# Kernel tuning notes

Measured on AMD Instinct MI355X. Metric: run time of the kernel, lower is better.

The kernel has to match this reference:

```python
import jax, jax.numpy as jnp
import numpy as np

N = 2_000_000   # num_nodes
C = 128         # in_channels
B = 256         # num graphs
K = 32          # max branches per graph (branch ids in [0, K))
NEG_SLOPE = 0.01  # torch leaky_relu default


def setup_inputs() -> dict:
    key = jax.random.key(0)
    k1, k2, k3, k4, k5, k6 = jax.random.split(key, 6)
    node_embed = jax.random.normal(k1, (N, C), dtype=jnp.float32)
    batch = jnp.sort(jax.random.randint(k2, (N,), 0, B, dtype=jnp.int64))
    branch = jax.random.randint(k3, (N,), 0, K, dtype=jnp.int64)
    s1 = 1.0 / np.sqrt(C)
    W1 = jax.random.uniform(k4, (C, C), jnp.float32, -s1, s1)
    b1 = jnp.zeros((C,), jnp.float32)
    W2 = jax.random.uniform(k5, (C, 1), jnp.float32, -s1, s1)
    b2 = jnp.zeros((1,), jnp.float32)
    return {"node_embed": node_embed, "batch": batch, "branch": branch,
            "W1": W1, "b1": b1, "W2": W2, "b2": b2}


def reference(node_embed, batch, branch, W1, b1, W2, b2):
    # Original code compacts branch ids via per-graph offsets (cumsum of max+1).
    # Equivalent static-shape formulation: global slot id = batch*K + branch,
    # and a per-graph mask keeping slots b <= max(branch in graph) — exactly the
    # branches 0..num_branch_per_graph-1 that repeat_interleave covers (including
    # empty branches below the max, whose pooled embed is 0 -> MLP(0)).
    gid = batch * K + branch                               # [N]
    branch_embed = jax.ops.segment_sum(node_embed, gid, num_segments=B * K)  # [B*K, C]
    h = branch_embed @ W1 + b1
    h = jnp.where(h >= 0, h, NEG_SLOPE * h)                # leaky_relu
    branch_value = h @ W2 + b2                             # [B*K, 1]
    max_b = jax.ops.segment_max(branch, batch, num_segments=B)  # [B]
    mask = (jnp.arange(K)[None, :] <= max_b[:, None]).astype(branch_value.dtype)  # [B, K]
    graph_value = jnp.sum(branch_value.reshape(B, K) * mask, axis=1, keepdims=True)  # [B, 1]
    return graph_value
```

## Files before the change

kernel.cpp:

```cpp
#include <hip/hip_runtime.h>

#define NCH 128
#define NGR 256
#define NBR 32
#define NEG_SLOPE 0.01f

typedef __attribute__((ext_vector_type(8))) short bf16x8;
typedef __attribute__((ext_vector_type(4))) float f32x4;

constexpr int TROWS = 32;

__device__ inline unsigned short rtne_bf16(float x) {
    unsigned u = __float_as_uint(x);
    return (unsigned short)((u + 0x7FFFu + ((u >> 16) & 1u)) >> 16);
}
__device__ inline unsigned pack_hl(float v) {
    const unsigned u = __float_as_uint(v);
    const unsigned short h = (unsigned short)(u >> 16);
    const float hf = __uint_as_float(u & 0xFFFF0000u);
    const unsigned short l = rtne_bf16(v - hf);
    return ((unsigned)h << 16) | (unsigned)l;
}

__global__ __launch_bounds__(512, 4) void scatter_mfma(
    const float* __restrict__ node_embed,
    const int*   __restrict__ batch,
    const int*   __restrict__ branch,
    float*       __restrict__ part,
    int*         __restrict__ max_b_part,
    int n_nodes)
{
    __shared__ float buf[3][TROWS][NCH] __attribute__((aligned(16)));
    __shared__ int   sbr_i[3][64]       __attribute__((aligned(16)));
    __shared__ int   seg_s[2];
    __shared__ int   wm[8];

    const int t    = threadIdx.x;
    const int bid  = blockIdx.x;
    const int g    = bid >> 1;
    const int half = bid & 1;
    const int wave = t >> 6;
    const int lane = t & 63;
    const int c    = wave;
    const int gq   = lane >> 4;
    const int m    = lane & 15;

    if (t < 2) {
        const int target = g + t;
        int lo = 0, hi = n_nodes;
        while (lo < hi) { int mid = (lo + hi) >> 1; if (batch[mid] < target) lo = mid + 1; else hi = mid; }
        seg_s[t] = lo;
    }
    __syncthreads();
    const int s0 = seg_s[0], s1 = seg_s[1];
    const int nt_tot = (s1 - s0 + TROWS - 1) / TROWS;
    const int ntA    = (nt_tot + 1) >> 1;
    const int sa     = half ? s0 + ntA * TROWS : s0;
    const int nt     = half ? nt_tot - ntA : ntA;

    auto stage = [&](int ti, int bi) {
        const int c0n = sa + ti * TROWS;
        #pragma unroll
        for (int u = 0; u < 2; ++u) {
            const int koff = (u * 8 + wave) * 1024;
            const int lanebyte = koff + lane * 16;
            const int rowg = c0n + (lanebyte >> 9);
            const char* src = (const char*)node_embed + ((size_t)c0n * 512 + (size_t)lanebyte);
            if (rowg >= s1) src = (const char*)node_embed;
            __builtin_amdgcn_global_load_lds(
                (const __attribute__((address_space(1))) void*)src,
                (__attribute__((address_space(3))) void*)((char*)&buf[bi][0][0] + koff),
                16, 0, 0);
        }
        if (wave == 0) {
            const int i0 = min(c0n + lane, n_nodes - 1);
            __builtin_amdgcn_global_load_lds(
                (const __attribute__((address_space(1))) void*)(branch + i0),
                (__attribute__((address_space(3))) void*)((char*)&sbr_i[bi][0]), 4, 0, 0);
        }
    };

    f32x4 acc0 = {0.f, 0.f, 0.f, 0.f};
    f32x4 acc1 = {0.f, 0.f, 0.f, 0.f};
    int mymax = -1;

    auto compute = [&](int ti, int bi) {
        const int rem = s1 - (sa + ti * TROWS);
        const int4 i0 = *(const int4*)&sbr_i[bi][gq * 8];
        const int4 i1 = *(const int4*)&sbr_i[bi][gq * 8 + 4];
        const int idv[8] = {i0.x, i0.y, i0.z, i0.w, i1.x, i1.y, i1.z, i1.w};
        bf16x8 a0, a1, bh, bl;
        #pragma unroll
        for (int j = 0; j < 8; ++j) {
            const float v = buf[bi][gq * 8 + j][c * 16 + m];
            const unsigned u = __float_as_uint(v);
            bh[j] = (short)(unsigned short)(u >> 16);
            const float hf = __uint_as_float(u & 0xFFFF0000u);
            bl[j] = (short)rtne_bf16(v - hf);
            const bool val = (gq * 8 + j) < rem;
            a0[j] = (val && idv[j] == m)      ? (short)0x3F80 : (short)0;
            a1[j] = (val && idv[j] == m + 16) ? (short)0x3F80 : (short)0;
            if (val) mymax = max(mymax, idv[j]);
        }
        acc0 = __builtin_amdgcn_mfma_f32_16x16x32_bf16(a0, bh, acc0, 0, 0, 0);
        acc0 = __builtin_amdgcn_mfma_f32_16x16x32_bf16(a0, bl, acc0, 0, 0, 0);
        acc1 = __builtin_amdgcn_mfma_f32_16x16x32_bf16(a1, bh, acc1, 0, 0, 0);
        acc1 = __builtin_amdgcn_mfma_f32_16x16x32_bf16(a1, bl, acc1, 0, 0, 0);
    };

    if (nt > 0) {
        stage(0, 0);
        if (nt > 1) stage(1, 1);
        if (nt > 1) {
            if (wave == 0) asm volatile("s_waitcnt vmcnt(3)" ::: "memory");
            else           asm volatile("s_waitcnt vmcnt(2)" ::: "memory");
        } else {
            asm volatile("s_waitcnt vmcnt(0)" ::: "memory");
        }
        __builtin_amdgcn_s_barrier();
        __builtin_amdgcn_sched_barrier(0);

        for (int ti = 0; ti < nt; ++ti) {
            const int bi = ti % 3;
            if (ti + 2 < nt) stage(ti + 2, (ti + 2) % 3);
            const int k = min(nt - 1 - ti, 2);
            if (wave == 0) {
                if (k == 2)      asm volatile("s_waitcnt vmcnt(6)" ::: "memory");
                else if (k == 1) asm volatile("s_waitcnt vmcnt(3)" ::: "memory");
                else             asm volatile("s_waitcnt vmcnt(0)" ::: "memory");
            } else {
                if (k == 2)      asm volatile("s_waitcnt vmcnt(4)" ::: "memory");
                else if (k == 1) asm volatile("s_waitcnt vmcnt(2)" ::: "memory");
                else             asm volatile("s_waitcnt vmcnt(0)" ::: "memory");
            }
            __builtin_amdgcn_s_barrier();
            __builtin_amdgcn_sched_barrier(0);
            compute(ti, bi);
            __builtin_amdgcn_s_barrier();
            __builtin_amdgcn_sched_barrier(0);
        }
    }

    {
        const int sr = gq * 4;
        float* be = part + (size_t)half * NGR * NBR * NCH
                  + (size_t)g * NBR * NCH + (size_t)c * 16 + m;
        #pragma unroll
        for (int r = 0; r < 4; ++r) {
            be[(sr + r) * NCH]      = acc0[r];
            be[(16 + sr + r) * NCH] = acc1[r];
        }
    }

    int v = mymax;
    #pragma unroll
    for (int off = 32; off > 0; off >>= 1) v = max(v, __shfl_down(v, off));
    if (lane == 0) wm[wave] = v;
    __syncthreads();
    if (t == 0) {
        int mb = wm[0];
        #pragma unroll
        for (int i = 1; i < 8; ++i) mb = max(mb, wm[i]);
        max_b_part[half * NGR + g] = mb;
    }
}

__global__ __launch_bounds__(512) void mlp_mfma(
    const float* __restrict__ part,
    const int*   __restrict__ max_b_part,
    const float* __restrict__ W1,
    const float* __restrict__ b1,
    const float* __restrict__ W2,
    const float* __restrict__ b2,
    float*       __restrict__ out)
{
    __shared__ unsigned w1p[128 * 130];
    __shared__ unsigned epk[32 * 132];
    __shared__ float    red[32 * 8];

    const int t    = threadIdx.x;
    const int g    = blockIdx.x;
    const int wave = t >> 6;
    const int lane = t & 63;
    const int gq   = lane >> 4;
    const int m    = lane & 15;
    const int sh   = wave & 1;
    const int c0   = wave >> 1;

    #pragma unroll
    for (int i = 0; i < 8; ++i) {
        const int eb  = i * 2048 + t * 4;
        const int row = eb >> 7, col = eb & 127;
        const float4 w = *(const float4*)&W1[eb];
        unsigned* d = &w1p[row * 130 + col];
        *(uint2*)d       = make_uint2(pack_hl(w.x), pack_hl(w.y));
        *(uint2*)(d + 2) = make_uint2(pack_hl(w.z), pack_hl(w.w));
    }
    {
        const int slot = t >> 4, kb = (t & 15) * 8;
        const size_t base = ((size_t)g * NBR + slot) * NCH + kb;
        const float* pB = part + (size_t)NGR * NBR * NCH;
        float4 e0 = *(const float4*)&part[base];
        float4 e1 = *(const float4*)&part[base + 4];
        const float4 f0 = *(const float4*)&pB[base];
        const float4 f1 = *(const float4*)&pB[base + 4];
        e0.x += f0.x; e0.y += f0.y; e0.z += f0.z; e0.w += f0.w;
        e1.x += f1.x; e1.y += f1.y; e1.z += f1.z; e1.w += f1.w;
        unsigned* d = &epk[slot * 132 + kb];
        *(uint4*)d       = make_uint4(pack_hl(e0.x), pack_hl(e0.y), pack_hl(e0.z), pack_hl(e0.w));
        *(uint4*)(d + 4) = make_uint4(pack_hl(e1.x), pack_hl(e1.y), pack_hl(e1.z), pack_hl(e1.w));
    }
    const float b1v0 = b1[c0 * 16 + m],      b1v1 = b1[(c0 + 4) * 16 + m];
    const float w2v0 = W2[c0 * 16 + m],      w2v1 = W2[(c0 + 4) * 16 + m];
    __syncthreads();

    f32x4 accA = {0.f, 0.f, 0.f, 0.f};
    f32x4 accB = {0.f, 0.f, 0.f, 0.f};
    #pragma unroll
    for (int ks = 0; ks < 4; ++ks) {
        const int k0 = ks * 32;
        const unsigned* ap = &epk[(sh * 16 + m) * 132 + k0 + gq * 8];
        const uint4 aw0 = *(const uint4*)ap;
        const uint4 aw1 = *(const uint4*)(ap + 4);
        const unsigned aw[8] = {aw0.x, aw0.y, aw0.z, aw0.w, aw1.x, aw1.y, aw1.z, aw1.w};
        bf16x8 ah, al;
        #pragma unroll
        for (int j = 0; j < 8; ++j) { ah[j] = (short)(aw[j] >> 16); al[j] = (short)(aw[j] & 0xFFFFu); }

        bf16x8 bh, blo;
        #pragma unroll
        for (int j = 0; j < 8; ++j) {
            const unsigned w = w1p[(k0 + gq * 8 + j) * 130 + c0 * 16 + m];
            bh[j] = (short)(w >> 16); blo[j] = (short)(w & 0xFFFFu);
        }
        accA = __builtin_amdgcn_mfma_f32_16x16x32_bf16(ah, bh,  accA, 0, 0, 0);
        accA = __builtin_amdgcn_mfma_f32_16x16x32_bf16(al, bh,  accA, 0, 0, 0);
        accA = __builtin_amdgcn_mfma_f32_16x16x32_bf16(ah, blo, accA, 0, 0, 0);

        #pragma unroll
        for (int j = 0; j < 8; ++j) {
            const unsigned w = w1p[(k0 + gq * 8 + j) * 130 + (c0 + 4) * 16 + m];
            bh[j] = (short)(w >> 16); blo[j] = (short)(w & 0xFFFFu);
        }
        accB = __builtin_amdgcn_mfma_f32_16x16x32_bf16(ah, bh,  accB, 0, 0, 0);
        accB = __builtin_amdgcn_mfma_f32_16x16x32_bf16(al, bh,  accB, 0, 0, 0);
        accB = __builtin_amdgcn_mfma_f32_16x16x32_bf16(ah, blo, accB, 0, 0, 0);
    }

    #pragma unroll
    for (int r = 0; r < 4; ++r) {
        float h0 = accA[r] + b1v0;
        h0 = (h0 >= 0.f) ? h0 : NEG_SLOPE * h0;
        float s0v = h0 * w2v0;
        float h1 = accB[r] + b1v1;
        h1 = (h1 >= 0.f) ? h1 : NEG_SLOPE * h1;
        float s1v = h1 * w2v1;
        #pragma unroll
        for (int off = 1; off < 16; off <<= 1) {
            s0v += __shfl_xor(s0v, off);
            s1v += __shfl_xor(s1v, off);
        }
        if (m == 0) {
            const int slot = sh * 16 + gq * 4 + r;
            red[slot * 8 + c0]     = s0v;
            red[slot * 8 + c0 + 4] = s1v;
        }
    }
    __syncthreads();

    if (t < 64) {
        const int rr = lane & 31;
        float v = 0.f;
        #pragma unroll
        for (int cc = 0; cc < 8; ++cc) v += red[rr * 8 + cc];
        const int mb = max(max_b_part[g], max_b_part[NGR + g]);
        float val = (lane < 32 && rr <= mb) ? (v + b2[0]) : 0.f;
        #pragma unroll
        for (int off = 32; off > 0; off >>= 1) val += __shfl_down(val, off);
        if (t == 0) out[g] = val;
    }
}

extern "C" void kernel_launch(void* const* d_in, const int* in_sizes, int n_in,
                              void* d_out, int out_size, void* d_ws, size_t ws_size,
                              hipStream_t stream) {
    const float* node_embed = (const float*)d_in[0];
    const int*   batch      = (const int*)d_in[1];
    const int*   branch     = (const int*)d_in[2];
    const float* W1         = (const float*)d_in[3];
    const float* b1         = (const float*)d_in[4];
    const float* W2         = (const float*)d_in[5];
    const float* b2         = (const float*)d_in[6];
    float*       out        = (float*)d_out;

    const int n_nodes = in_sizes[0] / NCH;

    float* part = (float*)d_ws;
    int*   max_b_part = (int*)((char*)d_ws + 2 * (size_t)NGR * NBR * NCH * sizeof(float));

    scatter_mfma<<<2 * NGR, 512, 0, stream>>>(node_embed, batch, branch,
                                              part, max_b_part, n_nodes);
    mlp_mfma<<<NGR, 512, 0, stream>>>(part, max_b_part, W1, b1, W2, b2, out);
}
```

Measured before the change: 210.0 us.

## Split each graph across four blocks and use double buffering to raise occupancy

Each graph's node range is now split across four blocks instead of two, giving 1024 scatter blocks. The shared-memory ring drops from three stages to two so more blocks can be resident, and launch bounds now request 6 blocks per CU. The MLP kernel sums four partial slabs and four max partials. The risk is a shallower prefetch depth per block and extra partial-sum traffic in the second kernel.

Result: slower. 234.3 us (+11.5%).

```diff
diff --git a/kernel.cpp b/kernel.cpp
--- a/kernel.cpp
+++ b/kernel.cpp
@@ -9,6 +9,7 @@
 typedef __attribute__((ext_vector_type(4))) float f32x4;
 
 constexpr int TROWS = 32;
+constexpr int NSPLIT = 4;
 
 __device__ inline unsigned short rtne_bf16(float x) {
     unsigned u = __float_as_uint(x);
@@ -22,7 +23,7 @@
     return ((unsigned)h << 16) | (unsigned)l;
 }
 
-__global__ __launch_bounds__(512, 4) void scatter_mfma(
+__global__ __launch_bounds__(512, 6) void scatter_mfma(
     const float* __restrict__ node_embed,
     const int*   __restrict__ batch,
     const int*   __restrict__ branch,
@@ -30,15 +31,15 @@
     int*         __restrict__ max_b_part,
     int n_nodes)
 {
-    __shared__ float buf[3][TROWS][NCH] __attribute__((aligned(16)));
-    __shared__ int   sbr_i[3][64]       __attribute__((aligned(16)));
+    __shared__ float buf[2][TROWS][NCH] __attribute__((aligned(16)));
+    __shared__ int   sbr_i[2][64]       __attribute__((aligned(16)));
     __shared__ int   seg_s[2];
     __shared__ int   wm[8];
 
     const int t    = threadIdx.x;
     const int bid  = blockIdx.x;
-    const int g    = bid >> 1;
-    const int half = bid & 1;
+    const int g    = bid >> 2;
+    const int q    = bid & 3;
     const int wave = t >> 6;
     const int lane = t & 63;
     const int c    = wave;
@@ -54,9 +55,11 @@
     __syncthreads();
     const int s0 = seg_s[0], s1 = seg_s[1];
     const int nt_tot = (s1 - s0 + TROWS - 1) / TROWS;
-    const int ntA    = (nt_tot + 1) >> 1;
-    const int sa     = half ? s0 + ntA * TROWS : s0;
-    const int nt     = half ? nt_tot - ntA : ntA;
+    const int per    = (nt_tot + NSPLIT - 1) / NSPLIT;
+    const int t0     = q * per;
+    const int t1     = min(t0 + per, nt_tot);
+    const int nt     = max(t1 - t0, 0);
+    const int sa     = s0 + t0 * TROWS;
 
     auto stage = [&](int ti, int bi) {
         const int c0n = sa + ti * TROWS;
@@ -110,28 +113,14 @@
 
     if (nt > 0) {
         stage(0, 0);
-        if (nt > 1) stage(1, 1);
-        if (nt > 1) {
-            if (wave == 0) asm volatile("s_waitcnt vmcnt(3)" ::: "memory");
-            else           asm volatile("s_waitcnt vmcnt(2)" ::: "memory");
-        } else {
-            asm volatile("s_waitcnt vmcnt(0)" ::: "memory");
-        }
-        __builtin_amdgcn_s_barrier();
-        __builtin_amdgcn_sched_barrier(0);
-
         for (int ti = 0; ti < nt; ++ti) {
-            const int bi = ti % 3;
-            if (ti + 2 < nt) stage(ti + 2, (ti + 2) % 3);
-            const int k = min(nt - 1 - ti, 2);
-            if (wave == 0) {
-                if (k == 2)      asm volatile("s_waitcnt vmcnt(6)" ::: "memory");
-                else if (k == 1) asm volatile("s_waitcnt vmcnt(3)" ::: "memory");
-                else             asm volatile("s_waitcnt vmcnt(0)" ::: "memory");
+            const int bi = ti & 1;
+            if (ti + 1 < nt) stage(ti + 1, bi ^ 1);
+            if (ti + 1 < nt) {
+                if (wave == 0) asm volatile("s_waitcnt vmcnt(3)" ::: "memory");
+                else           asm volatile("s_waitcnt vmcnt(2)" ::: "memory");
             } else {
-                if (k == 2)      asm volatile("s_waitcnt vmcnt(4)" ::: "memory");
-                else if (k == 1) asm volatile("s_waitcnt vmcnt(2)" ::: "memory");
-                else             asm volatile("s_waitcnt vmcnt(0)" ::: "memory");
+                asm volatile("s_waitcnt vmcnt(0)" ::: "memory");
             }
             __builtin_amdgcn_s_barrier();
             __builtin_amdgcn_sched_barrier(0);
@@ -143,7 +132,7 @@
 
     {
         const int sr = gq * 4;
-        float* be = part + (size_t)half * NGR * NBR * NCH
+        float* be = part + (size_t)q * NGR * NBR * NCH
                   + (size_t)g * NBR * NCH + (size_t)c * 16 + m;
         #pragma unroll
         for (int r = 0; r < 4; ++r) {
@@ -161,7 +150,7 @@
         int mb = wm[0];
         #pragma unroll
         for (int i = 1; i < 8; ++i) mb = max(mb, wm[i]);
-        max_b_part[half * NGR + g] = mb;
+        max_b_part[q * NGR + g] = mb;
     }
 }
 
@@ -199,13 +188,16 @@
     {
         const int slot = t >> 4, kb = (t & 15) * 8;
         const size_t base = ((size_t)g * NBR + slot) * NCH + kb;
-        const float* pB = part + (size_t)NGR * NBR * NCH;
+        const size_t pstride = (size_t)NGR * NBR * NCH;
         float4 e0 = *(const float4*)&part[base];
         float4 e1 = *(const float4*)&part[base + 4];
-        const float4 f0 = *(const float4*)&pB[base];
-        const float4 f1 = *(const float4*)&pB[base + 4];
-        e0.x += f0.x; e0.y += f0.y; e0.z += f0.z; e0.w += f0.w;
-        e1.x += f1.x; e1.y += f1.y; e1.z += f1.z; e1.w += f1.w;
+        #pragma unroll
+        for (int pp = 1; pp < NSPLIT; ++pp) {
+            const float4 f0 = *(const float4*)&part[pp * pstride + base];
+            const float4 f1 = *(const float4*)&part[pp * pstride + base + 4];
+            e0.x += f0.x; e0.y += f0.y; e0.z += f0.z; e0.w += f0.w;
+            e1.x += f1.x; e1.y += f1.y; e1.z += f1.z; e1.w += f1.w;
+        }
         unsigned* d = &epk[slot * 132 + kb];
         *(uint4*)d       = make_uint4(pack_hl(e0.x), pack_hl(e0.y), pack_hl(e0.z), pack_hl(e0.w));
         *(uint4*)(d + 4) = make_uint4(pack_hl(e1.x), pack_hl(e1.y), pack_hl(e1.z), pack_hl(e1.w));
@@ -273,7 +265,9 @@
         float v = 0.f;
         #pragma unroll
         for (int cc = 0; cc < 8; ++cc) v += red[rr * 8 + cc];
-        const int mb = max(max_b_part[g], max_b_part[NGR + g]);
+        int mb = max_b_part[g];
+        #pragma unroll
+        for (int pp = 1; pp < NSPLIT; ++pp) mb = max(mb, max_b_part[pp * NGR + g]);
         float val = (lane < 32 && rr <= mb) ? (v + b2[0]) : 0.f;
         #pragma unroll
         for (int off = 32; off > 0; off >>= 1) val += __shfl_down(val, off);
@@ -296,9 +290,10 @@
     const int n_nodes = in_sizes[0] / NCH;
 
     float* part = (float*)d_ws;
-    int*   max_b_part = (int*)((char*)d_ws + 2 * (size_t)NGR * NBR * NCH * sizeof(float));
-
-    scatter_mfma<<<2 * NGR, 512, 0, stream>>>(node_embed, batch, branch,
-                                              part, max_b_part, n_nodes);
+    int*   max_b_part = (int*)((char*)d_ws
+                       + (size_t)NSPLIT * NGR * NBR * NCH * sizeof(float));
+
+    scatter_mfma<<<NSPLIT * NGR, 512, 0, stream>>>(node_embed, batch, branch,
+                                                   part, max_b_part, n_nodes);
     mlp_mfma<<<NGR, 512, 0, stream>>>(part, max_b_part, W1, b1, W2, b2, out);
 }
```
